# Kernel tuning notes

Measured on AMD Instinct MI355X. Metric: run time of the kernel, lower is better.

## Reference

```python
import jax, jax.numpy as jnp
import numpy as np

TEMPERATURE = 8.0  # sqrt(head_dim=64)
NEG_INF = -1.0e9


def setup_inputs() -> dict:
    key = jax.random.key(0)
    kq, kk, kv, ks, km = jax.random.split(key, 5)
    B, H, S, D = 4, 8, 1024, 64
    q = jax.random.normal(kq, (B, H, S, D), dtype=jnp.float32)
    k = jax.random.normal(kk, (B, H, S, D), dtype=jnp.float32)
    v = jax.random.normal(kv, (B, H, S, D), dtype=jnp.float32)
    sph = jax.random.uniform(ks, (B, H, S, S), dtype=jnp.float32)
    mask = jax.random.randint(km, (B, 1, S, S), 0, 2, dtype=jnp.int32)
    return {"q": q, "k": k, "v": v, "sph": sph, "mask": mask}


def reference(q, k, v, sph, mask):
    # scores: [B,H,S,S]
    attn = jnp.einsum("bhqd,bhkd->bhqk", q / TEMPERATURE, k)
    attn = attn * sph
    attn = jnp.where(mask == 0, NEG_INF, attn)
    p_attn = jax.nn.softmax(attn, axis=-1)  # dropout in eval mode = identity
    output = jnp.einsum("bhqk,bhkd->bhqd", p_attn, v)
    return (output, p_attn)
```

## Files before the change

### kernel.cpp

```cpp
#include <hip/hip_runtime.h>

#define S_DIM 1024
#define TQ 16

typedef __attribute__((ext_vector_type(4))) float f32x4;
typedef __attribute__((ext_vector_type(4))) int i32x4;
typedef _Float16 half4 __attribute__((ext_vector_type(4)));
typedef _Float16 half8 __attribute__((ext_vector_type(8)));

__device__ inline half8 pack8h(f32x4 a, f32x4 b) {
  half8 r;
  r[0] = (_Float16)a.x; r[1] = (_Float16)a.y;
  r[2] = (_Float16)a.z; r[3] = (_Float16)a.w;
  r[4] = (_Float16)b.x; r[5] = (_Float16)b.y;
  r[6] = (_Float16)b.z; r[7] = (_Float16)b.w;
  return r;
}

__global__ __launch_bounds__(256)
void prep_kernel(const float* __restrict__ kp, const float* __restrict__ vp,
                 _Float16* __restrict__ k16, _Float16* __restrict__ vt16)
{
  __shared__ _Float16 tile[64][72];
  const int tid = threadIdx.x;
  const int bh  = blockIdx.x >> 4;
  const int c0  = (blockIdx.x & 15) * 64;
  const size_t base = ((size_t)bh * S_DIM + c0) * 64;

  #pragma unroll
  for (int i = 0; i < 4; ++i) {
    const int idx = i * 256 + tid;
    f32x4 kv = *(const f32x4*)(kp + base + (size_t)idx * 4);
    half4 h; h[0] = (_Float16)kv.x; h[1] = (_Float16)kv.y;
    h[2] = (_Float16)kv.z; h[3] = (_Float16)kv.w;
    *(half4*)(k16 + base + (size_t)idx * 4) = h;
  }
  #pragma unroll
  for (int i = 0; i < 4; ++i) {
    const int idx = i * 256 + tid;
    const int r = idx >> 4, c4 = idx & 15;
    f32x4 vv = *(const f32x4*)(vp + base + (size_t)r * 64 + c4 * 4);
    tile[c4 * 4 + 0][r] = (_Float16)vv.x;
    tile[c4 * 4 + 1][r] = (_Float16)vv.y;
    tile[c4 * 4 + 2][r] = (_Float16)vv.z;
    tile[c4 * 4 + 3][r] = (_Float16)vv.w;
  }
  __syncthreads();
  #pragma unroll
  for (int i = 0; i < 2; ++i) {
    const int idx = i * 256 + tid;
    const int d = idx >> 3, g = idx & 7;
    half8 h = *(half8*)&tile[d][g * 8];
    *(half8*)(vt16 + ((size_t)bh * 64 + d) * S_DIM + c0 + g * 8) = h;
  }
}

__global__ __launch_bounds__(256, 4)
void sdpa_kernel(const float* __restrict__ qp,
                 const _Float16* __restrict__ k16,
                 const _Float16* __restrict__ vt16,
                 const float* __restrict__ sphp,
                 const int* __restrict__ maskp,
                 float* __restrict__ outp, float* __restrict__ pp)
{
  __shared__ _Float16 pb[TQ][1032];
  __shared__ float    red[4][16];

  const int tid   = threadIdx.x;
  const int lane  = tid & 63;
  const int wave  = tid >> 6;
  const int row16 = lane & 15;
  const int quad  = lane >> 4;

  const int bh = blockIdx.x >> 6;
  const int qt = blockIdx.x & 63;
  const int b  = bh >> 3;
  const int q0 = qt * TQ;
  const size_t bhS = (size_t)bh * S_DIM;

  const float* qrow = qp + (bhS + q0 + row16) * 64 + quad * 8;
  const f32x4 s8 = {0.125f, 0.125f, 0.125f, 0.125f};
  f32x4 qa = *(const f32x4*)(qrow);
  f32x4 qb = *(const f32x4*)(qrow + 4);
  f32x4 qc = *(const f32x4*)(qrow + 32);
  f32x4 qd = *(const f32x4*)(qrow + 36);
  const half8 bq0 = pack8h(qa * s8, qb * s8);
  const half8 bq1 = pack8h(qc * s8, qd * s8);

  const int kb = wave * 256;
  const _Float16* kbp = k16 + (bhS + kb) * 64;
  #pragma unroll
  for (int t = 0; t < 16; ++t) {
    const _Float16* krow = kbp + (t * 16 + row16) * 64 + quad * 8;
    half8 a0 = *(const half8*)(krow);
    half8 a1 = *(const half8*)(krow + 32);
    f32x4 acc = {0.f, 0.f, 0.f, 0.f};
    acc = __builtin_amdgcn_mfma_f32_16x16x32_f16(a0, bq0, acc, 0, 0, 0);
    acc = __builtin_amdgcn_mfma_f32_16x16x32_f16(a1, bq1, acc, 0, 0, 0);
    half4 hv; hv[0] = (_Float16)acc.x; hv[1] = (_Float16)acc.y;
    hv[2] = (_Float16)acc.z; hv[3] = (_Float16)acc.w;
    *(half4*)&pb[row16][kb + t * 16 + quad * 4] = hv;
  }

  const int kcol = kb + lane * 4;
  #pragma unroll
  for (int r = 0; r < TQ; ++r) {
    const size_t rowoff = (bhS + q0 + r) * S_DIM + kcol;
    f32x4 p4 = __builtin_nontemporal_load((const f32x4*)(sphp + rowoff));
    i32x4 m4 = *(const i32x4*)(maskp + (((size_t)b * S_DIM + q0 + r) * S_DIM + kcol));
    half4 sh = *(half4*)&pb[r][kcol];
    f32x4 e;
    e.x = (m4.x == 0) ? 0.f : __expf((float)sh[0] * p4.x);
    e.y = (m4.y == 0) ? 0.f : __expf((float)sh[1] * p4.y);
    e.z = (m4.z == 0) ? 0.f : __expf((float)sh[2] * p4.z);
    e.w = (m4.w == 0) ? 0.f : __expf((float)sh[3] * p4.w);
    half4 hv; hv[0] = (_Float16)e.x; hv[1] = (_Float16)e.y;
    hv[2] = (_Float16)e.z; hv[3] = (_Float16)e.w;
    *(half4*)&pb[r][kcol] = hv;
    float sum = (e.x + e.y) + (e.z + e.w);
    #pragma unroll
    for (int off = 32; off > 0; off >>= 1)
      sum += __shfl_xor(sum, off);
    if (lane == 0) red[wave][r] = sum;
  }
  __syncthreads();

  #pragma unroll
  for (int r = 0; r < TQ; ++r) {
    const float inv = 1.0f / ((red[0][r] + red[1][r]) + (red[2][r] + red[3][r]));
    half4 e = *(half4*)&pb[r][kcol];
    f32x4 pv;
    pv.x = (float)e[0] * inv; pv.y = (float)e[1] * inv;
    pv.z = (float)e[2] * inv; pv.w = (float)e[3] * inv;
    __builtin_nontemporal_store(pv, (f32x4*)(pp + (bhS + q0 + r) * S_DIM + kcol));
  }

  f32x4 oacc = {0.f, 0.f, 0.f, 0.f};
  const _Float16* vrow = vt16 + ((size_t)bh * 64 + wave * 16 + row16) * S_DIM + quad * 8;
  #pragma unroll 8
  for (int c = 0; c < 32; ++c) {
    half8 af = *(const half8*)(vrow + c * 32);
    half8 bf = *(const half8*)&pb[row16][c * 32 + quad * 8];
    oacc = __builtin_amdgcn_mfma_f32_16x16x32_f16(af, bf, oacc, 0, 0, 0);
  }

  const float ssum = (red[0][row16] + red[1][row16]) + (red[2][row16] + red[3][row16]);
  const float invq = 1.0f / ssum;
  float* orow = outp + (bhS + q0 + row16) * 64 + wave * 16 + quad * 4;
  *(f32x4*)orow = oacc * invq;
}

extern "C" void kernel_launch(void* const* d_in, const int* in_sizes, int n_in,
                              void* d_out, int out_size, void* d_ws, size_t ws_size,
                              hipStream_t stream) {
  const float* q    = (const float*)d_in[0];
  const float* k    = (const float*)d_in[1];
  const float* v    = (const float*)d_in[2];
  const float* sph  = (const float*)d_in[3];
  const int*   mask = (const int*)d_in[4];
  float* out  = (float*)d_out;
  float* patt = out + (size_t)4 * 8 * 1024 * 64;

  _Float16* k16  = (_Float16*)d_ws;
  _Float16* vt16 = k16 + (size_t)32 * S_DIM * 64;

  hipLaunchKernelGGL(prep_kernel, dim3(32 * 16), dim3(256), 0, stream,
                     k, v, k16, vt16);
  hipLaunchKernelGGL(sdpa_kernel, dim3(32 * 64), dim3(256), 0, stream,
                     q, k16, vt16, sph, mask, out, patt);
}
```

Baseline: 316.9 us.

## Bit-pack mask once, prefetch sph rows early, use exp2 and rcp

A new pre-pass packs the int32 mask into bitmasks with wave ballots, so the attention kernel reads 1 bit per element instead of 4 bytes. That removes the redundant 8x mask reread across heads. The sph rows are now loaded at kernel start, before the QK MFMA, so their latency overlaps compute. The softmax loop now handles 8 columns per lane across two rows at a time. Scores are pre-scaled by log2(e) so exp2f can be used, and divisions become rcp. Costs are an extra kernel launch and more workspace, plus more registers held for the prefetched sph.

```diff
diff --git a/kernel.cpp b/kernel.cpp
--- a/kernel.cpp
+++ b/kernel.cpp
@@ -2,6 +2,7 @@
 
 #define S_DIM 1024
 #define TQ 16
+#define LOG2E 1.44269504f
 
 typedef __attribute__((ext_vector_type(4))) float f32x4;
 typedef __attribute__((ext_vector_type(4))) int i32x4;
@@ -55,12 +56,32 @@
   }
 }
 
+__global__ __launch_bounds__(256)
+void maskpack_kernel(const int* __restrict__ maskp, unsigned int* __restrict__ pm)
+{
+  const int tid  = threadIdx.x;
+  const int lane = tid & 63;
+  const int wave = tid >> 6;
+  const int row  = blockIdx.x;
+  const size_t base = (size_t)row * S_DIM + wave * 256;
+  unsigned long long bal0, bal1, bal2, bal3;
+  bal0 = __ballot(maskp[base +   0 + lane] != 0);
+  bal1 = __ballot(maskp[base +  64 + lane] != 0);
+  bal2 = __ballot(maskp[base + 128 + lane] != 0);
+  bal3 = __ballot(maskp[base + 192 + lane] != 0);
+  if (lane == 0) {
+    unsigned long long* dst =
+        (unsigned long long*)(pm + (size_t)row * 32 + wave * 8);
+    dst[0] = bal0; dst[1] = bal1; dst[2] = bal2; dst[3] = bal3;
+  }
+}
+
 __global__ __launch_bounds__(256, 4)
 void sdpa_kernel(const float* __restrict__ qp,
                  const _Float16* __restrict__ k16,
                  const _Float16* __restrict__ vt16,
                  const float* __restrict__ sphp,
-                 const int* __restrict__ maskp,
+                 const unsigned int* __restrict__ pm,
                  float* __restrict__ outp, float* __restrict__ pp)
 {
   __shared__ _Float16 pb[TQ][1032];
@@ -77,6 +98,25 @@
   const int b  = bh >> 3;
   const int q0 = qt * TQ;
   const size_t bhS = (size_t)bh * S_DIM;
+
+  const int kb = wave * 256;
+  const int ll = lane & 31;
+  const int lh = lane >> 5;
+  const int kcol2 = kb + ll * 8;
+
+  const unsigned int* pmbase = pm + ((size_t)b * S_DIM + q0) * 32 + wave * 8 + (ll >> 2);
+  unsigned int mb[8];
+  #pragma unroll
+  for (int i = 0; i < 8; ++i) mb[i] = pmbase[(size_t)(2 * i + lh) * 32];
+  const int msh = (ll & 3) * 8;
+
+  f32x4 sA[4][2], sB[4][2];
+  #pragma unroll
+  for (int i = 0; i < 4; ++i) {
+    const float* p = sphp + (bhS + q0 + 2 * i + lh) * S_DIM + kcol2;
+    sA[i][0] = __builtin_nontemporal_load((const f32x4*)p);
+    sA[i][1] = __builtin_nontemporal_load((const f32x4*)(p + 4));
+  }
 
   const float* qrow = qp + (bhS + q0 + row16) * 64 + quad * 8;
   const f32x4 s8 = {0.125f, 0.125f, 0.125f, 0.125f};
@@ -87,7 +127,6 @@
   const half8 bq0 = pack8h(qa * s8, qb * s8);
   const half8 bq1 = pack8h(qc * s8, qd * s8);
 
-  const int kb = wave * 256;
   const _Float16* kbp = k16 + (bhS + kb) * 64;
   #pragma unroll
   for (int t = 0; t < 16; ++t) {
@@ -97,42 +136,68 @@
     f32x4 acc = {0.f, 0.f, 0.f, 0.f};
     acc = __builtin_amdgcn_mfma_f32_16x16x32_f16(a0, bq0, acc, 0, 0, 0);
     acc = __builtin_amdgcn_mfma_f32_16x16x32_f16(a1, bq1, acc, 0, 0, 0);
-    half4 hv; hv[0] = (_Float16)acc.x; hv[1] = (_Float16)acc.y;
-    hv[2] = (_Float16)acc.z; hv[3] = (_Float16)acc.w;
+    half4 hv;
+    hv[0] = (_Float16)(acc.x * LOG2E); hv[1] = (_Float16)(acc.y * LOG2E);
+    hv[2] = (_Float16)(acc.z * LOG2E); hv[3] = (_Float16)(acc.w * LOG2E);
     *(half4*)&pb[row16][kb + t * 16 + quad * 4] = hv;
   }
 
-  const int kcol = kb + lane * 4;
-  #pragma unroll
-  for (int r = 0; r < TQ; ++r) {
-    const size_t rowoff = (bhS + q0 + r) * S_DIM + kcol;
-    f32x4 p4 = __builtin_nontemporal_load((const f32x4*)(sphp + rowoff));
-    i32x4 m4 = *(const i32x4*)(maskp + (((size_t)b * S_DIM + q0 + r) * S_DIM + kcol));
-    half4 sh = *(half4*)&pb[r][kcol];
-    f32x4 e;
-    e.x = (m4.x == 0) ? 0.f : __expf((float)sh[0] * p4.x);
-    e.y = (m4.y == 0) ? 0.f : __expf((float)sh[1] * p4.y);
-    e.z = (m4.z == 0) ? 0.f : __expf((float)sh[2] * p4.z);
-    e.w = (m4.w == 0) ? 0.f : __expf((float)sh[3] * p4.w);
-    half4 hv; hv[0] = (_Float16)e.x; hv[1] = (_Float16)e.y;
-    hv[2] = (_Float16)e.z; hv[3] = (_Float16)e.w;
-    *(half4*)&pb[r][kcol] = hv;
-    float sum = (e.x + e.y) + (e.z + e.w);
+  auto proc = [&](int i, const f32x4* sv, unsigned int mbi) {
+    const int r = 2 * i + lh;
+    half8 sh = *(half8*)&pb[r][kcol2];
+    const unsigned int m = (mbi >> msh) & 0xFFu;
+    float x0 = (float)sh[0] * sv[0].x, x1 = (float)sh[1] * sv[0].y;
+    float x2 = (float)sh[2] * sv[0].z, x3 = (float)sh[3] * sv[0].w;
+    float x4 = (float)sh[4] * sv[1].x, x5 = (float)sh[5] * sv[1].y;
+    float x6 = (float)sh[6] * sv[1].z, x7 = (float)sh[7] * sv[1].w;
+    float e0 = (m &   1u) ? __builtin_amdgcn_exp2f(x0) : 0.f;
+    float e1 = (m &   2u) ? __builtin_amdgcn_exp2f(x1) : 0.f;
+    float e2 = (m &   4u) ? __builtin_amdgcn_exp2f(x2) : 0.f;
+    float e3 = (m &   8u) ? __builtin_amdgcn_exp2f(x3) : 0.f;
+    float e4 = (m &  16u) ? __builtin_amdgcn_exp2f(x4) : 0.f;
+    float e5 = (m &  32u) ? __builtin_amdgcn_exp2f(x5) : 0.f;
+    float e6 = (m &  64u) ? __builtin_amdgcn_exp2f(x6) : 0.f;
+    float e7 = (m & 128u) ? __builtin_amdgcn_exp2f(x7) : 0.f;
+    half8 hv;
+    hv[0] = (_Float16)e0; hv[1] = (_Float16)e1;
+    hv[2] = (_Float16)e2; hv[3] = (_Float16)e3;
+    hv[4] = (_Float16)e4; hv[5] = (_Float16)e5;
+    hv[6] = (_Float16)e6; hv[7] = (_Float16)e7;
+    *(half8*)&pb[r][kcol2] = hv;
+    float sum = ((e0 + e1) + (e2 + e3)) + ((e4 + e5) + (e6 + e7));
     #pragma unroll
-    for (int off = 32; off > 0; off >>= 1)
+    for (int off = 16; off > 0; off >>= 1)
       sum += __shfl_xor(sum, off);
-    if (lane == 0) red[wave][r] = sum;
-  }
+    if (ll == 0) red[wave][r] = sum;
+  };
+
+  #pragma unroll
+  for (int i = 0; i < 4; ++i) {
+    const float* p = sphp + (bhS + q0 + 8 + 2 * i + lh) * S_DIM + kcol2;
+    sB[i][0] = __builtin_nontemporal_load((const f32x4*)p);
+    sB[i][1] = __builtin_nontemporal_load((const f32x4*)(p + 4));
+  }
+  #pragma unroll
+  for (int i = 0; i < 4; ++i) proc(i, sA[i], mb[i]);
+  #pragma unroll
+  for (int i = 0; i < 4; ++i) proc(4 + i, sB[i], mb[4 + i]);
+
   __syncthreads();
 
   #pragma unroll
-  for (int r = 0; r < TQ; ++r) {
-    const float inv = 1.0f / ((red[0][r] + red[1][r]) + (red[2][r] + red[3][r]));
-    half4 e = *(half4*)&pb[r][kcol];
-    f32x4 pv;
-    pv.x = (float)e[0] * inv; pv.y = (float)e[1] * inv;
-    pv.z = (float)e[2] * inv; pv.w = (float)e[3] * inv;
-    __builtin_nontemporal_store(pv, (f32x4*)(pp + (bhS + q0 + r) * S_DIM + kcol));
+  for (int i = 0; i < 8; ++i) {
+    const int r = 2 * i + lh;
+    const float inv = __builtin_amdgcn_rcpf(
+        (red[0][r] + red[1][r]) + (red[2][r] + red[3][r]));
+    half8 e = *(half8*)&pb[r][kcol2];
+    f32x4 p0, p1;
+    p0.x = (float)e[0] * inv; p0.y = (float)e[1] * inv;
+    p0.z = (float)e[2] * inv; p0.w = (float)e[3] * inv;
+    p1.x = (float)e[4] * inv; p1.y = (float)e[5] * inv;
+    p1.z = (float)e[6] * inv; p1.w = (float)e[7] * inv;
+    float* dst = pp + (bhS + q0 + r) * S_DIM + kcol2;
+    __builtin_nontemporal_store(p0, (f32x4*)dst);
+    __builtin_nontemporal_store(p1, (f32x4*)(dst + 4));
   }
 
   f32x4 oacc = {0.f, 0.f, 0.f, 0.f};
@@ -145,7 +210,7 @@
   }
 
   const float ssum = (red[0][row16] + red[1][row16]) + (red[2][row16] + red[3][row16]);
-  const float invq = 1.0f / ssum;
+  const float invq = __builtin_amdgcn_rcpf(ssum);
   float* orow = outp + (bhS + q0 + row16) * 64 + wave * 16 + quad * 4;
   *(f32x4*)orow = oacc * invq;
 }
@@ -163,9 +228,12 @@
 
   _Float16* k16  = (_Float16*)d_ws;
   _Float16* vt16 = k16 + (size_t)32 * S_DIM * 64;
-
+  unsigned int* pm = (unsigned int*)(vt16 + (size_t)32 * S_DIM * 64);
+
+  hipLaunchKernelGGL(maskpack_kernel, dim3(4 * S_DIM), dim3(256), 0, stream,
+                     mask, pm);
   hipLaunchKernelGGL(prep_kernel, dim3(32 * 16), dim3(256), 0, stream,
                      k, v, k16, vt16);
   hipLaunchKernelGGL(sdpa_kernel, dim3(32 * 64), dim3(256), 0, stream,
-                     q, k16, vt16, sph, mask, out, patt);
-}
+                     q, k16, vt16, sph, pm, out, patt);
+}
```

Measured after the change: 320.6 us. About the same (+1.2%).
